# Kernel optimization log

Hardware: AMD Instinct MI355X
Metric: run time of the kernel (lower is better)

The kernel has to match this reference:

```python
import jax, jax.numpy as jnp
import numpy as np

N_NODES = 50000
N_EDGES = 400000
D_IN = 256
EMBED = 256
HEADS = 8
HEAD_DIM = EMBED // HEADS

def mish(x):
    return x * jnp.tanh(jax.nn.softplus(x))

def setup_inputs() -> dict:
    key = jax.random.key(0)
    ks = jax.random.split(key, 8)
    nodes = jax.random.normal(ks[0], (N_NODES, D_IN), dtype=jnp.float32)
    senders = jax.random.randint(ks[1], (N_EDGES,), 0, N_NODES, dtype=jnp.int32)
    receivers = jax.random.randint(ks[2], (N_EDGES,), 0, N_NODES, dtype=jnp.int32)
    s = 1.0 / np.sqrt(D_IN)
    Wi = jax.random.normal(ks[3], (D_IN, HEADS, HEAD_DIM), dtype=jnp.float32) * s
    bi = jnp.zeros((HEADS, HEAD_DIM), dtype=jnp.float32)
    Wj = jax.random.normal(ks[4], (D_IN, HEADS, HEAD_DIM), dtype=jnp.float32) * s
    bj = jnp.zeros((HEADS, HEAD_DIM), dtype=jnp.float32)
    a_w = jax.random.normal(ks[5], (HEAD_DIM,), dtype=jnp.float32) / np.sqrt(HEAD_DIM)
    a_b = jnp.zeros((), dtype=jnp.float32)
    return {"nodes": nodes, "senders": senders, "receivers": receivers,
            "Wi": Wi, "bi": bi, "Wj": Wj, "bj": bj, "a_w": a_w, "a_b": a_b}

def reference(nodes, senders, receivers, Wi, bi, Wj, bj, a_w, a_b):
    n = nodes.shape[0]
    # gather + per-edge projections: [E, H, hd]
    sent = jnp.einsum('ed,dhk->ehk', nodes[senders], Wi) + bi
    recv = jnp.einsum('ed,dhk->ehk', nodes[receivers], Wj) + bj
    # attention logit MLP: mish(add) then Dense(1) (kernel shared across heads)
    x = mish(sent + recv)
    logits = jnp.einsum('ehk,k->eh', x, a_w) + a_b  # [E, H]
    # segment softmax over incoming edges of each receiver
    maxs = jax.ops.segment_max(logits, receivers, num_segments=n)  # [N, H]
    unnorm = jnp.exp(logits - maxs[receivers])
    denom = jax.ops.segment_sum(unnorm, receivers, num_segments=n)  # [N, H]
    weights = unnorm / denom[receivers]  # [E, H]
    # weighted message aggregation
    messages = sent * weights[:, :, None]  # [E, H, hd]
    out = jax.ops.segment_sum(messages, receivers, num_segments=n)  # [N, H, hd]
    return out.reshape(n, -1)  # [N, embed_dim]
```

## Files before the change

kernel.cpp:

```cpp
#include <hip/hip_runtime.h>
#include <hip/hip_bf16.h>
#include <math.h>

#define DIM 256
#define HEADS 8
#define HEAD_DIM 32

typedef short  s16x8 __attribute__((ext_vector_type(8)));
typedef float  f32x4 __attribute__((ext_vector_type(4)));

__device__ __forceinline__ unsigned short f2bf_rne(float f) {
  unsigned int b = __builtin_bit_cast(unsigned int, f);
  b = (b + 0x7FFFu + ((b >> 16) & 1u)) >> 16;
  return (unsigned short)b;
}
__device__ __forceinline__ float bf2f(unsigned short s) {
  unsigned int b = ((unsigned int)s) << 16;
  return __builtin_bit_cast(float, b);
}

__global__ __launch_bounds__(256) void wtrans_kernel(
    const float* __restrict__ Wi, const float* __restrict__ Wj,
    short* __restrict__ Wt_ih, short* __restrict__ Wt_il,
    short* __restrict__ Wt_jh, short* __restrict__ Wt_jl) {
  const int n = blockIdx.x & 255;
  const float* W = (blockIdx.x < 256) ? Wi : Wj;
  short* Th = (blockIdx.x < 256) ? Wt_ih : Wt_jh;
  short* Tl = (blockIdx.x < 256) ? Wt_il : Wt_jl;
  const int k = threadIdx.x;
  float f = W[k * 256 + n];
  unsigned short hb = f2bf_rne(f);
  unsigned short lb = f2bf_rne(f - bf2f(hb));
  Th[n * 256 + k] = (short)hb;
  Tl[n * 256 + k] = (short)lb;
}

__global__ __launch_bounds__(256, 4) void proj2_mfma_kernel(
    const float* __restrict__ nodes,
    const short* __restrict__ Wt_ih, const short* __restrict__ Wt_il,
    const short* __restrict__ Wt_jh, const short* __restrict__ Wt_jl,
    const float* __restrict__ bi, const float* __restrict__ bj,
    float* __restrict__ Pi, float* __restrict__ Pj, int M) {
  __shared__ __align__(16) short Ah[32 * 256];
  __shared__ __align__(16) short Al[32 * 256];
  const int t = threadIdx.x;
  const int row0 = blockIdx.x * 32;

  const float4* n4 = (const float4*)nodes;
  #pragma unroll
  for (int i = 0; i < 8; ++i) {
    int u = t + i * 256;
    int r = u >> 6;
    int q = u & 63;
    int gr = row0 + r;
    float4 v = make_float4(0.f, 0.f, 0.f, 0.f);
    if (gr < M) v = n4[(size_t)gr * 64 + q];
    float fv[4] = {v.x, v.y, v.z, v.w};
    short hv[4], lv[4];
    #pragma unroll
    for (int j = 0; j < 4; ++j) {
      unsigned short hb = f2bf_rne(fv[j]);
      hv[j] = (short)hb;
      lv[j] = (short)f2bf_rne(fv[j] - bf2f(hb));
    }
    int boff = r * 512 + ((q * 8) ^ ((r & 7) << 4));
    *(short4*)((char*)Ah + boff) = make_short4(hv[0], hv[1], hv[2], hv[3]);
    *(short4*)((char*)Al + boff) = make_short4(lv[0], lv[1], lv[2], lv[3]);
  }
  __syncthreads();

  const int lane = t & 63, cg = t >> 6;
  const int l15 = lane & 15;
  const int kq = lane >> 4;

  #pragma unroll
  for (int pass = 0; pass < 2; ++pass) {
    const short* Wth = pass ? Wt_jh : Wt_ih;
    const short* Wtl = pass ? Wt_jl : Wt_il;
    const float* bias = pass ? bj : bi;
    float* P = pass ? Pj : Pi;

    f32x4 acc[2][4];
    #pragma unroll
    for (int mt = 0; mt < 2; ++mt)
      #pragma unroll
      for (int nt = 0; nt < 4; ++nt) acc[mt][nt] = (f32x4){0.f, 0.f, 0.f, 0.f};

    #pragma unroll
    for (int c = 0; c < 8; ++c) {
      s16x8 Ahf[2], Alf[2];
      #pragma unroll
      for (int mt = 0; mt < 2; ++mt) {
        int lr = mt * 16 + l15;
        int boff = lr * 512 + ((c * 64 + kq * 16) ^ ((lr & 7) << 4));
        Ahf[mt] = *(const s16x8*)((const char*)Ah + boff);
        Alf[mt] = *(const s16x8*)((const char*)Al + boff);
      }
      #pragma unroll
      for (int nt = 0; nt < 4; ++nt) {
        int col = cg * 64 + nt * 16 + l15;
        const short* wb = Wth + col * 256 + c * 32 + kq * 8;
        const short* wl = Wtl + col * 256 + c * 32 + kq * 8;
        s16x8 bh = *(const s16x8*)wb;
        s16x8 bl = *(const s16x8*)wl;
        #pragma unroll
        for (int mt = 0; mt < 2; ++mt) {
          acc[mt][nt] = __builtin_amdgcn_mfma_f32_16x16x32_bf16(Ahf[mt], bh, acc[mt][nt], 0, 0, 0);
          acc[mt][nt] = __builtin_amdgcn_mfma_f32_16x16x32_bf16(Alf[mt], bh, acc[mt][nt], 0, 0, 0);
          acc[mt][nt] = __builtin_amdgcn_mfma_f32_16x16x32_bf16(Ahf[mt], bl, acc[mt][nt], 0, 0, 0);
        }
      }
    }

    #pragma unroll
    for (int nt = 0; nt < 4; ++nt) {
      int col = cg * 64 + nt * 16 + l15;
      float bv = bias[col];
      #pragma unroll
      for (int mt = 0; mt < 2; ++mt) {
        #pragma unroll
        for (int j = 0; j < 4; ++j) {
          int gr = row0 + mt * 16 + kq * 4 + j;
          if (gr < M) P[(size_t)gr * 256 + col] = acc[mt][nt][j] + bv;
        }
      }
    }
  }
}

__global__ void hist_kernel(const int* __restrict__ recv, int* __restrict__ cnt,
                            int E) {
  int e = blockIdx.x * 256 + threadIdx.x;
  if (e < E) atomicAdd(&cnt[recv[e]], 1);
}

__device__ __forceinline__ int block_scan256(int x, int t, int* wsum) {
  const int lane = t & 63, wid = t >> 6;
  #pragma unroll
  for (int d = 1; d < 64; d <<= 1) {
    int y = __shfl_up(x, (unsigned)d);
    if (lane >= d) x += y;
  }
  if (lane == 63) wsum[wid] = x;
  __syncthreads();
  int add = 0;
  if (wid > 0) add += wsum[0];
  if (wid > 1) add += wsum[1];
  if (wid > 2) add += wsum[2];
  x += add;
  __syncthreads();
  return x;
}

__global__ __launch_bounds__(256) void scanA_kernel(const int* __restrict__ cnt,
                                                    int* __restrict__ offs,
                                                    int* __restrict__ bsum,
                                                    int n) {
  __shared__ int wsum[4];
  const int t = threadIdx.x;
  const int i = blockIdx.x * 256 + t;
  int x = (i < n) ? cnt[i] : 0;
  int s = block_scan256(x, t, wsum);
  if (i < n) offs[i + 1] = s;
  if (t == 255) bsum[blockIdx.x] = s;
  if (t == 0 && blockIdx.x == 0) offs[0] = 0;
}

__global__ __launch_bounds__(256) void scanB_kernel(const int* __restrict__ bsum,
                                                    int* __restrict__ bbase,
                                                    int nb) {
  __shared__ int wsum[4];
  __shared__ int carry_s;
  const int t = threadIdx.x;
  if (t == 0) carry_s = 0;
  __syncthreads();
  for (int base = 0; base < nb; base += 256) {
    int i = base + t;
    int x = (i < nb) ? bsum[i] : 0;
    int s = block_scan256(x, t, wsum);
    int c = carry_s;
    if (i < nb) bbase[i] = c + s - x;
    __syncthreads();
    if (t == 255) carry_s = c + s;
    __syncthreads();
  }
}

__global__ __launch_bounds__(256) void scanC_kernel(int* __restrict__ offs,
                                                    const int* __restrict__ bbase,
                                                    int n) {
  const int i = blockIdx.x * 256 + threadIdx.x;
  if (i < n) offs[i + 1] += bbase[blockIdx.x];
}

__global__ void scatter_kernel(const int* __restrict__ recv,
                               const int* __restrict__ snd,
                               const int* __restrict__ offs,
                               int* __restrict__ cursor,
                               int* __restrict__ sorted_snd, int E) {
  int e = blockIdx.x * 256 + threadIdx.x;
  if (e < E) {
    int r = recv[e];
    int slot = offs[r] + atomicAdd(&cursor[r], 1);
    sorted_snd[slot] = snd[e];
  }
}

__device__ __forceinline__ float mish_f(float x) {
  float t = __expf(fminf(x, 40.f));
  float u = t * (t + 2.f);
  return x * u * __builtin_amdgcn_rcpf(u + 2.f);
}

__global__ __launch_bounds__(256) void node_kernel(
    const float* __restrict__ Pi, const float* __restrict__ Pj,
    const int* __restrict__ offs, const int* __restrict__ sorted_snd,
    const float* __restrict__ a_w, const float* __restrict__ a_b,
    float* __restrict__ out, int n) {
  const int wid = threadIdx.x >> 6, lane = threadIdx.x & 63;
  const int r = blockIdx.x * 4 + wid;
  if (r >= n) return;

  const int beg = offs[r], end = offs[r + 1];
  const float4* Pi4 = (const float4*)Pi;
  const float4* Pj4 = (const float4*)Pj;

  const float4 pj = Pj4[r * 64 + lane];
  const float4 aw = ((const float4*)a_w)[lane & 7];
  const float ab = a_b[0];

  float4 acc = make_float4(0.f, 0.f, 0.f, 0.f);
  float m = -INFINITY, denom = 0.f;

  float4 p0 = make_float4(0.f, 0.f, 0.f, 0.f), p1 = p0, p2 = p0;
  if (beg < end)     p0 = Pi4[(size_t)sorted_snd[beg] * 64 + lane];
  if (beg + 1 < end) p1 = Pi4[(size_t)sorted_snd[beg + 1] * 64 + lane];
  if (beg + 2 < end) p2 = Pi4[(size_t)sorted_snd[beg + 2] * 64 + lane];

  for (int idx = beg; idx < end; ++idx) {
    float4 pi = p0;
    p0 = p1; p1 = p2;
    if (idx + 3 < end)
      p2 = Pi4[(size_t)sorted_snd[idx + 3] * 64 + lane];

    float partial;
    partial  = mish_f(pi.x + pj.x) * aw.x;
    partial += mish_f(pi.y + pj.y) * aw.y;
    partial += mish_f(pi.z + pj.z) * aw.z;
    partial += mish_f(pi.w + pj.w) * aw.w;
    partial += __shfl_xor(partial, 1);
    partial += __shfl_xor(partial, 2);
    partial += __shfl_xor(partial, 4);

    float lo = partial + ab;
    float mn = fmaxf(m, lo);
    float scale = __expf(m - mn);
    float p = __expf(lo - mn);
    denom = denom * scale + p;
    acc.x = acc.x * scale + p * pi.x;
    acc.y = acc.y * scale + p * pi.y;
    acc.z = acc.z * scale + p * pi.z;
    acc.w = acc.w * scale + p * pi.w;
    m = mn;
  }

  float inv = (end > beg) ? 1.f / denom : 0.f;
  float4 o = make_float4(acc.x * inv, acc.y * inv, acc.z * inv, acc.w * inv);
  ((float4*)out)[r * 64 + lane] = o;
}

extern "C" void kernel_launch(void* const* d_in, const int* in_sizes, int n_in,
                              void* d_out, int out_size, void* d_ws,
                              size_t ws_size, hipStream_t stream) {
  const float* nodes = (const float*)d_in[0];
  const int* senders = (const int*)d_in[1];
  const int* receivers = (const int*)d_in[2];
  const float* Wi = (const float*)d_in[3];
  const float* bi = (const float*)d_in[4];
  const float* Wj = (const float*)d_in[5];
  const float* bj = (const float*)d_in[6];
  const float* a_w = (const float*)d_in[7];
  const float* a_b = (const float*)d_in[8];
  float* out = (float*)d_out;

  const int N = in_sizes[0] / DIM;
  const int E = in_sizes[1];
  const int nb = (N + 255) / 256;

  char* ws = (char*)d_ws;
  float* Pi = (float*)ws;
  float* Pj = Pi + (size_t)N * DIM;
  int* cnt = (int*)(Pj + (size_t)N * DIM);
  int* cursor = cnt + N;
  int* offs = cursor + N;
  int* bsum = offs + N + 1;
  int* bbase = bsum + nb;
  int* sorted_snd = bbase + nb;
  short* Wt_ih = (short*)(((uintptr_t)sorted_snd + 15) & ~(uintptr_t)15);
  short* Wt_il = Wt_ih + 65536;
  short* Wt_jh = Wt_il + 65536;
  short* Wt_jl = Wt_jh + 65536;

  hipMemsetAsync(cnt, 0, (size_t)2 * N * sizeof(int), stream);

  wtrans_kernel<<<512, 256, 0, stream>>>(Wi, Wj, Wt_ih, Wt_il, Wt_jh, Wt_jl);
  proj2_mfma_kernel<<<(N + 31) / 32, 256, 0, stream>>>(
      nodes, Wt_ih, Wt_il, Wt_jh, Wt_jl, bi, bj, Pi, Pj, N);

  hist_kernel<<<(E + 255) / 256, 256, 0, stream>>>(receivers, cnt, E);
  scanA_kernel<<<nb, 256, 0, stream>>>(cnt, offs, bsum, N);
  scanB_kernel<<<1, 256, 0, stream>>>(bsum, bbase, nb);
  scanC_kernel<<<nb, 256, 0, stream>>>(offs, bbase, N);
  scatter_kernel<<<(E + 255) / 256, 256, 0, stream>>>(receivers, senders, offs,
                                                      cursor, sorted_snd, E);

  node_kernel<<<(N + 3) / 4, 256, 0, stream>>>(Pi, Pj, offs, sorted_snd, a_w,
                                               a_b, out, N);
}
```

Baseline: 356.5 us.

## Interleave hi/lo weight layout, double-buffer B fragments, fold scan fixup into consumers

The transposed bf16 hi and lo weight splits are stored interleaved in one buffer, so each lane reads its hi and lo fragments from adjacent addresses. The GEMM loop prefetches the next K-chunk's B fragments into registers while the current chunk's MFMAs run. The scanC launch is removed: scatter and node kernels now add the block base offset on the fly when reading offsets. This saves a launch and a pass over offsets, at the cost of extra registers in the GEMM and an extra load per offset lookup.

Result: slower. 418.3 us (+17.3%).

```diff
diff --git a/kernel.cpp b/kernel.cpp
--- a/kernel.cpp
+++ b/kernel.cpp
@@ -21,24 +21,23 @@
 
 __global__ __launch_bounds__(256) void wtrans_kernel(
     const float* __restrict__ Wi, const float* __restrict__ Wj,
-    short* __restrict__ Wt_ih, short* __restrict__ Wt_il,
-    short* __restrict__ Wt_jh, short* __restrict__ Wt_jl) {
+    short* __restrict__ Wt_i, short* __restrict__ Wt_j) {
   const int n = blockIdx.x & 255;
   const float* W = (blockIdx.x < 256) ? Wi : Wj;
-  short* Th = (blockIdx.x < 256) ? Wt_ih : Wt_jh;
-  short* Tl = (blockIdx.x < 256) ? Wt_il : Wt_jl;
+  short* T = (blockIdx.x < 256) ? Wt_i : Wt_j;
   const int k = threadIdx.x;
   float f = W[k * 256 + n];
   unsigned short hb = f2bf_rne(f);
   unsigned short lb = f2bf_rne(f - bf2f(hb));
-  Th[n * 256 + k] = (short)hb;
-  Tl[n * 256 + k] = (short)lb;
+  const int c = k >> 5, r5 = k & 31, kq = r5 >> 3, j = r5 & 7;
+  const int base = n * 512 + c * 64 + kq * 16;
+  T[base + j] = (short)hb;
+  T[base + 8 + j] = (short)lb;
 }
 
 __global__ __launch_bounds__(256, 4) void proj2_mfma_kernel(
     const float* __restrict__ nodes,
-    const short* __restrict__ Wt_ih, const short* __restrict__ Wt_il,
-    const short* __restrict__ Wt_jh, const short* __restrict__ Wt_jl,
+    const short* __restrict__ Wt_i, const short* __restrict__ Wt_j,
     const float* __restrict__ bi, const float* __restrict__ bj,
     float* __restrict__ Pi, float* __restrict__ Pj, int M) {
   __shared__ __align__(16) short Ah[32 * 256];
@@ -75,8 +74,7 @@
 
   #pragma unroll
   for (int pass = 0; pass < 2; ++pass) {
-    const short* Wth = pass ? Wt_jh : Wt_ih;
-    const short* Wtl = pass ? Wt_jl : Wt_il;
+    const short* Wt = pass ? Wt_j : Wt_i;
     const float* bias = pass ? bj : bi;
     float* P = pass ? Pj : Pi;
 
@@ -86,8 +84,26 @@
       #pragma unroll
       for (int nt = 0; nt < 4; ++nt) acc[mt][nt] = (f32x4){0.f, 0.f, 0.f, 0.f};
 
+    s16x8 Bh[2][4], Bl[2][4];
+    #pragma unroll
+    for (int nt = 0; nt < 4; ++nt) {
+      const short* p = Wt + (cg * 64 + nt * 16 + l15) * 512 + kq * 16;
+      Bh[0][nt] = *(const s16x8*)p;
+      Bl[0][nt] = *(const s16x8*)(p + 8);
+    }
+
     #pragma unroll
     for (int c = 0; c < 8; ++c) {
+      const int cur = c & 1, nxt = cur ^ 1;
+      if (c + 1 < 8) {
+        #pragma unroll
+        for (int nt = 0; nt < 4; ++nt) {
+          const short* p = Wt + (cg * 64 + nt * 16 + l15) * 512 +
+                           (c + 1) * 64 + kq * 16;
+          Bh[nxt][nt] = *(const s16x8*)p;
+          Bl[nxt][nt] = *(const s16x8*)(p + 8);
+        }
+      }
       s16x8 Ahf[2], Alf[2];
       #pragma unroll
       for (int mt = 0; mt < 2; ++mt) {
@@ -98,16 +114,11 @@
       }
       #pragma unroll
       for (int nt = 0; nt < 4; ++nt) {
-        int col = cg * 64 + nt * 16 + l15;
-        const short* wb = Wth + col * 256 + c * 32 + kq * 8;
-        const short* wl = Wtl + col * 256 + c * 32 + kq * 8;
-        s16x8 bh = *(const s16x8*)wb;
-        s16x8 bl = *(const s16x8*)wl;
         #pragma unroll
         for (int mt = 0; mt < 2; ++mt) {
-          acc[mt][nt] = __builtin_amdgcn_mfma_f32_16x16x32_bf16(Ahf[mt], bh, acc[mt][nt], 0, 0, 0);
-          acc[mt][nt] = __builtin_amdgcn_mfma_f32_16x16x32_bf16(Alf[mt], bh, acc[mt][nt], 0, 0, 0);
-          acc[mt][nt] = __builtin_amdgcn_mfma_f32_16x16x32_bf16(Ahf[mt], bl, acc[mt][nt], 0, 0, 0);
+          acc[mt][nt] = __builtin_amdgcn_mfma_f32_16x16x32_bf16(Ahf[mt], Bh[cur][nt], acc[mt][nt], 0, 0, 0);
+          acc[mt][nt] = __builtin_amdgcn_mfma_f32_16x16x32_bf16(Alf[mt], Bh[cur][nt], acc[mt][nt], 0, 0, 0);
+          acc[mt][nt] = __builtin_amdgcn_mfma_f32_16x16x32_bf16(Ahf[mt], Bl[cur][nt], acc[mt][nt], 0, 0, 0);
         }
       }
     }
@@ -186,22 +197,21 @@
   }
 }
 
-__global__ __launch_bounds__(256) void scanC_kernel(int* __restrict__ offs,
-                                                    const int* __restrict__ bbase,
-                                                    int n) {
-  const int i = blockIdx.x * 256 + threadIdx.x;
-  if (i < n) offs[i + 1] += bbase[blockIdx.x];
+__device__ __forceinline__ int final_off(const int* __restrict__ offs_p,
+                                         const int* __restrict__ bbase, int m) {
+  return offs_p[m] + (m > 0 ? bbase[(m - 1) >> 8] : 0);
 }
 
 __global__ void scatter_kernel(const int* __restrict__ recv,
                                const int* __restrict__ snd,
-                               const int* __restrict__ offs,
+                               const int* __restrict__ offs_p,
+                               const int* __restrict__ bbase,
                                int* __restrict__ cursor,
                                int* __restrict__ sorted_snd, int E) {
   int e = blockIdx.x * 256 + threadIdx.x;
   if (e < E) {
     int r = recv[e];
-    int slot = offs[r] + atomicAdd(&cursor[r], 1);
+    int slot = final_off(offs_p, bbase, r) + atomicAdd(&cursor[r], 1);
     sorted_snd[slot] = snd[e];
   }
 }
@@ -214,14 +224,16 @@
 
 __global__ __launch_bounds__(256) void node_kernel(
     const float* __restrict__ Pi, const float* __restrict__ Pj,
-    const int* __restrict__ offs, const int* __restrict__ sorted_snd,
+    const int* __restrict__ offs_p, const int* __restrict__ bbase,
+    const int* __restrict__ sorted_snd,
     const float* __restrict__ a_w, const float* __restrict__ a_b,
     float* __restrict__ out, int n) {
   const int wid = threadIdx.x >> 6, lane = threadIdx.x & 63;
   const int r = blockIdx.x * 4 + wid;
   if (r >= n) return;
 
-  const int beg = offs[r], end = offs[r + 1];
+  const int beg = final_off(offs_p, bbase, r);
+  const int end = final_off(offs_p, bbase, r + 1);
   const float4* Pi4 = (const float4*)Pi;
   const float4* Pj4 = (const float4*)Pj;
 
@@ -296,24 +308,21 @@
   int* bsum = offs + N + 1;
   int* bbase = bsum + nb;
   int* sorted_snd = bbase + nb;
-  short* Wt_ih = (short*)(((uintptr_t)sorted_snd + 15) & ~(uintptr_t)15);
-  short* Wt_il = Wt_ih + 65536;
-  short* Wt_jh = Wt_il + 65536;
-  short* Wt_jl = Wt_jh + 65536;
+  short* Wt_i = (short*)(((uintptr_t)sorted_snd + 15) & ~(uintptr_t)15);
+  short* Wt_j = Wt_i + 256 * 512;
 
   hipMemsetAsync(cnt, 0, (size_t)2 * N * sizeof(int), stream);
 
-  wtrans_kernel<<<512, 256, 0, stream>>>(Wi, Wj, Wt_ih, Wt_il, Wt_jh, Wt_jl);
+  wtrans_kernel<<<512, 256, 0, stream>>>(Wi, Wj, Wt_i, Wt_j);
   proj2_mfma_kernel<<<(N + 31) / 32, 256, 0, stream>>>(
-      nodes, Wt_ih, Wt_il, Wt_jh, Wt_jl, bi, bj, Pi, Pj, N);
+      nodes, Wt_i, Wt_j, bi, bj, Pi, Pj, N);
 
   hist_kernel<<<(E + 255) / 256, 256, 0, stream>>>(receivers, cnt, E);
   scanA_kernel<<<nb, 256, 0, stream>>>(cnt, offs, bsum, N);
   scanB_kernel<<<1, 256, 0, stream>>>(bsum, bbase, nb);
-  scanC_kernel<<<nb, 256, 0, stream>>>(offs, bbase, N);
-  scatter_kernel<<<(E + 255) / 256, 256, 0, stream>>>(receivers, senders, offs,
-                                                      cursor, sorted_snd, E);
-
-  node_kernel<<<(N + 3) / 4, 256, 0, stream>>>(Pi, Pj, offs, sorted_snd, a_w,
-                                               a_b, out, N);
-}
+  scatter_kernel<<<(E + 255) / 256, 256, 0, stream>>>(
+      receivers, senders, offs, bbase, cursor, sorted_snd, E);
+
+  node_kernel<<<(N + 3) / 4, 256, 0, stream>>>(Pi, Pj, offs, bbase, sorted_snd,
+                                               a_w, a_b, out, N);
+}
```
